# Kernel tuning notes

Measured on AMD Instinct MI355X. Metric: run time of the kernel, lower is better.

Reference implementation:

```python
import jax, jax.numpy as jnp
import numpy as np

B = 8192
D_IN = 512
UNITS = 512


def setup_inputs() -> dict:
    key = jax.random.key(0)
    ks = jax.random.split(key, 9)
    sx = 1.0 / np.sqrt(D_IN)
    sh = 1.0 / np.sqrt(UNITS)
    return {
        "input_x": jax.random.normal(ks[0], (B, D_IN), jnp.float32),
        "input_h": jax.random.normal(ks[1], (B, UNITS), jnp.float32),
        "attention_score": jax.random.uniform(ks[2], (B, 1), jnp.float32),
        "Wx_r": jax.random.normal(ks[3], (D_IN, UNITS), jnp.float32) * sx,
        "b_r": jnp.zeros((UNITS,), jnp.float32),
        "Wh_r": jax.random.normal(ks[4], (UNITS, UNITS), jnp.float32) * sh,
        "Wx_u": jax.random.normal(ks[5], (D_IN, UNITS), jnp.float32) * sx,
        "b_u": jnp.zeros((UNITS,), jnp.float32),
        "Wh_u": jax.random.normal(ks[6], (UNITS, UNITS), jnp.float32) * sh,
        "Wx_h": jax.random.normal(ks[7], (D_IN, UNITS), jnp.float32) * sx,
        "b_h": jnp.zeros((UNITS,), jnp.float32),
        "Wh_h": jax.random.normal(ks[8], (UNITS, UNITS), jnp.float32) * sh,
    }


def reference(input_x, input_h, attention_score,
              Wx_r, b_r, Wh_r,
              Wx_u, b_u, Wh_u,
              Wx_h, b_h, Wh_h):
    # reset gate: sigmoid(Dense_b(x) + Dense(h))
    r = jax.nn.sigmoid(input_x @ Wx_r + b_r + input_h @ Wh_r)
    # update gate: sigmoid(Dense_b(x) + Dense(h))
    u = jax.nn.sigmoid(input_x @ Wx_u + b_u + input_h @ Wh_u)
    # candidate: tanh(Dense_b(x) + r * Dense(h))
    cal_h = jnp.tanh(input_x @ Wx_h + b_h + r * (input_h @ Wh_h))
    # attention-modulated update and interpolation
    u_att = attention_score * u
    h = (1.0 - u_att) * input_h + u_att * cal_h
    return h
```

## Files before the change

kernel.cpp:

```cpp
#include <hip/hip_runtime.h>
#include <hip/hip_bf16.h>

typedef __bf16 bf16x8 __attribute__((ext_vector_type(8)));
typedef float f32x4 __attribute__((ext_vector_type(4)));
typedef unsigned short us8 __attribute__((ext_vector_type(8)));

#define MFMA16 __builtin_amdgcn_mfma_f32_16x16x32_bf16

__device__ __forceinline__ unsigned short f2bf(float f) {
    unsigned int u = __float_as_uint(f);
    u += 0x7fffu + ((u >> 16) & 1u);
    return (unsigned short)(u >> 16);
}

__device__ __forceinline__ void gload_lds16(const void* g, void* l) {
    __builtin_amdgcn_global_load_lds(
        (const __attribute__((address_space(1))) unsigned int*)g,
        (__attribute__((address_space(3))) unsigned int*)l, 16, 0, 0);
}

__global__ void cvt_xh_kernel(const float* __restrict__ x, const float* __restrict__ h,
                              unsigned short* __restrict__ XP, unsigned short* __restrict__ HP) {
    int c = blockIdx.x * 256 + threadIdx.x;
    const float* src = (c >> 19) ? h : x;
    unsigned short* dst = (c >> 19) ? HP : XP;
    int c2 = c & 524287;
    int mb = c2 >> 10, kb = (c2 >> 6) & 15, lane = c2 & 63;
    int r = lane & 15, ko = lane >> 4;
    const float* p = src + (size_t)(mb * 16 + r) * 512 + kb * 32 + ko * 8;
    float4 v0 = *(const float4*)p;
    float4 v1 = *(const float4*)(p + 4);
    us8 o = { f2bf(v0.x), f2bf(v0.y), f2bf(v0.z), f2bf(v0.w),
              f2bf(v1.x), f2bf(v1.y), f2bf(v1.z), f2bf(v1.w) };
    *(us8*)(dst + (size_t)c2 * 8) = o;
}

__global__ void cvt_w_kernel(const float* __restrict__ W0, const float* __restrict__ W1,
                             const float* __restrict__ W2, const float* __restrict__ W3,
                             const float* __restrict__ W4, const float* __restrict__ W5,
                             unsigned short* __restrict__ WP) {
    int c = blockIdx.x * 256 + threadIdx.x;
    int w = c >> 15;
    const float* Wsrc;
    switch (w) {
        case 0: Wsrc = W0; break;
        case 1: Wsrc = W1; break;
        case 2: Wsrc = W2; break;
        case 3: Wsrc = W3; break;
        case 4: Wsrc = W4; break;
        default: Wsrc = W5; break;
    }
    int c2 = c & 32767;
    int nb = c2 >> 10, kb = (c2 >> 6) & 15, lane = c2 & 63;
    int cc = lane & 15, ko = lane >> 4;
    int kbase = kb * 32 + ko * 8;
    us8 o;
#pragma unroll
    for (int e = 0; e < 8; ++e)
        o[e] = f2bf(Wsrc[(size_t)(kbase + e) * 512 + nb * 16 + cc]);
    *(us8*)(WP + (size_t)c * 8) = o;
}

__global__ __launch_bounds__(256, 2) void augru_mm(
    const unsigned short* __restrict__ XP,
    const unsigned short* __restrict__ HP,
    const unsigned short* __restrict__ WP,
    const float* __restrict__ b_r, const float* __restrict__ b_u, const float* __restrict__ b_h,
    const float* __restrict__ att, const float* __restrict__ h32,
    float* __restrict__ out) {
    __shared__ unsigned char sB[2][12 * 1024];

    const int t = threadIdx.x;
    const int wv = t >> 6, lane = t & 63;
    const size_t laneoff = (size_t)lane * 16;

    const int bid = blockIdx.x;
    const int W = (bid & 7) * 64 + (bid >> 3);
    const int mblk = W >> 4, nblk = W & 15;
    const int nbase = nblk * 2;
    const int mbase = mblk * 16 + wv * 4;

    f32x4 accR[4][2] = {}, accU[4][2] = {}, accXH[4][2] = {}, accHH[4][2] = {};

    const unsigned char* pX[4];
    const unsigned char* pH[4];
#pragma unroll
    for (int mf = 0; mf < 4; ++mf) {
        size_t fb = ((size_t)(mbase + mf) * 16) << 10;
        pX[mf] = (const unsigned char*)XP + fb + laneoff;
        pH[mf] = (const unsigned char*)HP + fb + laneoff;
    }

#pragma unroll
    for (int i = 0; i < 3; ++i) {
        int s = wv * 3 + i;
        int w = s >> 1, nf = s & 1;
        const unsigned char* src = (const unsigned char*)WP +
            ((((size_t)(w * 32 + nbase + nf)) * 16 + 0) << 10) + laneoff;
        gload_lds16(src, &sB[0][s << 10]);
    }
    __syncthreads();

    int buf = 0;
    for (int kb = 0; kb < 16; ++kb) {
        bf16x8 ax[4], ah[4];
#pragma unroll
        for (int mf = 0; mf < 4; ++mf) {
            ax[mf] = *(const bf16x8*)(pX[mf] + ((size_t)kb << 10));
            ah[mf] = *(const bf16x8*)(pH[mf] + ((size_t)kb << 10));
        }
        if (kb < 15) {
#pragma unroll
            for (int i = 0; i < 3; ++i) {
                int s = wv * 3 + i;
                int w = s >> 1, nf = s & 1;
                const unsigned char* src = (const unsigned char*)WP +
                    ((((size_t)(w * 32 + nbase + nf)) * 16 + (kb + 1)) << 10) + laneoff;
                gload_lds16(src, &sB[buf ^ 1][s << 10]);
            }
        }
        bf16x8 bw[6][2];
#pragma unroll
        for (int s = 0; s < 12; ++s)
            bw[s >> 1][s & 1] = *(const bf16x8*)&sB[buf][(s << 10) + laneoff];
#pragma unroll
        for (int mf = 0; mf < 4; ++mf) {
#pragma unroll
            for (int nf = 0; nf < 2; ++nf) {
                accR[mf][nf]  = MFMA16(ax[mf], bw[0][nf], accR[mf][nf], 0, 0, 0);
                accR[mf][nf]  = MFMA16(ah[mf], bw[1][nf], accR[mf][nf], 0, 0, 0);
                accU[mf][nf]  = MFMA16(ax[mf], bw[2][nf], accU[mf][nf], 0, 0, 0);
                accU[mf][nf]  = MFMA16(ah[mf], bw[3][nf], accU[mf][nf], 0, 0, 0);
                accXH[mf][nf] = MFMA16(ax[mf], bw[4][nf], accXH[mf][nf], 0, 0, 0);
                accHH[mf][nf] = MFMA16(ah[mf], bw[5][nf], accHH[mf][nf], 0, 0, 0);
            }
        }
        __syncthreads();
        buf ^= 1;
    }

    const int lr = lane & 15, lg = lane >> 4;
#pragma unroll
    for (int nf = 0; nf < 2; ++nf) {
        const int col = nblk * 32 + nf * 16 + lr;
        const float br = b_r[col], bu = b_u[col], bh = b_h[col];
#pragma unroll
        for (int mf = 0; mf < 4; ++mf) {
            const int rowb = mblk * 256 + wv * 64 + mf * 16 + lg * 4;
#pragma unroll
            for (int q = 0; q < 4; ++q) {
                const int row = rowb + q;
                float r = 1.f / (1.f + __expf(-(accR[mf][nf][q] + br)));
                float u = 1.f / (1.f + __expf(-(accU[mf][nf][q] + bu)));
                float ph = accXH[mf][nf][q] + bh + r * accHH[mf][nf][q];
                ph = fminf(fmaxf(ph, -15.f), 15.f);
                float e = __expf(2.f * ph);
                float cal = (e - 1.f) / (e + 1.f);
                float hv = h32[(size_t)row * 512 + col];
                float ua = att[row] * u;
                out[(size_t)row * 512 + col] = fmaf(ua, cal - hv, hv);
            }
        }
    }
}

extern "C" void kernel_launch(void* const* d_in, const int* in_sizes, int n_in,
                              void* d_out, int out_size, void* d_ws, size_t ws_size,
                              hipStream_t stream) {
    const float* x    = (const float*)d_in[0];
    const float* h    = (const float*)d_in[1];
    const float* att  = (const float*)d_in[2];
    const float* Wx_r = (const float*)d_in[3];
    const float* b_r  = (const float*)d_in[4];
    const float* Wh_r = (const float*)d_in[5];
    const float* Wx_u = (const float*)d_in[6];
    const float* b_u  = (const float*)d_in[7];
    const float* Wh_u = (const float*)d_in[8];
    const float* Wx_h = (const float*)d_in[9];
    const float* b_h  = (const float*)d_in[10];
    const float* Wh_h = (const float*)d_in[11];
    float* out = (float*)d_out;

    unsigned short* XP = (unsigned short*)d_ws;
    unsigned short* HP = XP + 8192 * 512;
    unsigned short* WP = HP + 8192 * 512;

    cvt_xh_kernel<<<4096, 256, 0, stream>>>(x, h, XP, HP);
    cvt_w_kernel<<<768, 256, 0, stream>>>(Wx_r, Wh_r, Wx_u, Wh_u, Wx_h, Wh_h, WP);
    augru_mm<<<512, 256, 0, stream>>>(XP, HP, WP, b_r, b_u, b_h, att, h, out);
}
```

Before: 56.23 us.

## Merge conversion kernels and software-pipeline A-fragment loads in GEMM loop

Combines the activation and weight bf16 conversion kernels into one launch, removing one kernel launch and its tail. In the main GEMM, the K loop is unrolled by two with double-buffered register A fragments, so global loads of the next X/H fragments are issued before the current MFMAs instead of right before use. This hides global load latency but raises register pressure under the 2-blocks-per-CU launch bound.

```diff
diff --git a/kernel.cpp b/kernel.cpp
--- a/kernel.cpp
+++ b/kernel.cpp
@@ -19,46 +19,47 @@
         (__attribute__((address_space(3))) unsigned int*)l, 16, 0, 0);
 }
 
-__global__ void cvt_xh_kernel(const float* __restrict__ x, const float* __restrict__ h,
-                              unsigned short* __restrict__ XP, unsigned short* __restrict__ HP) {
-    int c = blockIdx.x * 256 + threadIdx.x;
-    const float* src = (c >> 19) ? h : x;
-    unsigned short* dst = (c >> 19) ? HP : XP;
-    int c2 = c & 524287;
-    int mb = c2 >> 10, kb = (c2 >> 6) & 15, lane = c2 & 63;
-    int r = lane & 15, ko = lane >> 4;
-    const float* p = src + (size_t)(mb * 16 + r) * 512 + kb * 32 + ko * 8;
-    float4 v0 = *(const float4*)p;
-    float4 v1 = *(const float4*)(p + 4);
-    us8 o = { f2bf(v0.x), f2bf(v0.y), f2bf(v0.z), f2bf(v0.w),
-              f2bf(v1.x), f2bf(v1.y), f2bf(v1.z), f2bf(v1.w) };
-    *(us8*)(dst + (size_t)c2 * 8) = o;
-}
-
-__global__ void cvt_w_kernel(const float* __restrict__ W0, const float* __restrict__ W1,
-                             const float* __restrict__ W2, const float* __restrict__ W3,
-                             const float* __restrict__ W4, const float* __restrict__ W5,
-                             unsigned short* __restrict__ WP) {
-    int c = blockIdx.x * 256 + threadIdx.x;
-    int w = c >> 15;
-    const float* Wsrc;
-    switch (w) {
-        case 0: Wsrc = W0; break;
-        case 1: Wsrc = W1; break;
-        case 2: Wsrc = W2; break;
-        case 3: Wsrc = W3; break;
-        case 4: Wsrc = W4; break;
-        default: Wsrc = W5; break;
+__global__ void cvt_all_kernel(const float* __restrict__ x, const float* __restrict__ h,
+                               unsigned short* __restrict__ XP, unsigned short* __restrict__ HP,
+                               const float* __restrict__ W0, const float* __restrict__ W1,
+                               const float* __restrict__ W2, const float* __restrict__ W3,
+                               const float* __restrict__ W4, const float* __restrict__ W5,
+                               unsigned short* __restrict__ WP) {
+    if (blockIdx.x < 4096) {
+        int c = blockIdx.x * 256 + threadIdx.x;
+        const float* src = (c >> 19) ? h : x;
+        unsigned short* dst = (c >> 19) ? HP : XP;
+        int c2 = c & 524287;
+        int mb = c2 >> 10, kb = (c2 >> 6) & 15, lane = c2 & 63;
+        int r = lane & 15, ko = lane >> 4;
+        const float* p = src + (size_t)(mb * 16 + r) * 512 + kb * 32 + ko * 8;
+        float4 v0 = *(const float4*)p;
+        float4 v1 = *(const float4*)(p + 4);
+        us8 o = { f2bf(v0.x), f2bf(v0.y), f2bf(v0.z), f2bf(v0.w),
+                  f2bf(v1.x), f2bf(v1.y), f2bf(v1.z), f2bf(v1.w) };
+        *(us8*)(dst + (size_t)c2 * 8) = o;
+    } else {
+        int c = (blockIdx.x - 4096) * 256 + threadIdx.x;
+        int w = c >> 15;
+        const float* Wsrc;
+        switch (w) {
+            case 0: Wsrc = W0; break;
+            case 1: Wsrc = W1; break;
+            case 2: Wsrc = W2; break;
+            case 3: Wsrc = W3; break;
+            case 4: Wsrc = W4; break;
+            default: Wsrc = W5; break;
+        }
+        int c2 = c & 32767;
+        int nb = c2 >> 10, kb = (c2 >> 6) & 15, lane = c2 & 63;
+        int cc = lane & 15, ko = lane >> 4;
+        int kbase = kb * 32 + ko * 8;
+        us8 o;
+#pragma unroll
+        for (int e = 0; e < 8; ++e)
+            o[e] = f2bf(Wsrc[(size_t)(kbase + e) * 512 + nb * 16 + cc]);
+        *(us8*)(WP + (size_t)c * 8) = o;
     }
-    int c2 = c & 32767;
-    int nb = c2 >> 10, kb = (c2 >> 6) & 15, lane = c2 & 63;
-    int cc = lane & 15, ko = lane >> 4;
-    int kbase = kb * 32 + ko * 8;
-    us8 o;
-#pragma unroll
-    for (int e = 0; e < 8; ++e)
-        o[e] = f2bf(Wsrc[(size_t)(kbase + e) * 512 + nb * 16 + cc]);
-    *(us8*)(WP + (size_t)c * 8) = o;
 }
 
 __global__ __launch_bounds__(256, 2) void augru_mm(
@@ -90,53 +91,57 @@
         pX[mf] = (const unsigned char*)XP + fb + laneoff;
         pH[mf] = (const unsigned char*)HP + fb + laneoff;
     }
-
+    const unsigned char* pW[3];
+    unsigned lds_off[3];
 #pragma unroll
     for (int i = 0; i < 3; ++i) {
         int s = wv * 3 + i;
         int w = s >> 1, nf = s & 1;
-        const unsigned char* src = (const unsigned char*)WP +
-            ((((size_t)(w * 32 + nbase + nf)) * 16 + 0) << 10) + laneoff;
-        gload_lds16(src, &sB[0][s << 10]);
+        pW[i] = (const unsigned char*)WP + (((size_t)(w * 32 + nbase + nf) * 16) << 10) + laneoff;
+        lds_off[i] = s << 10;
     }
+
+#define STAGE_B(kb1, bufi) \
+    { _Pragma("unroll") for (int i = 0; i < 3; ++i) \
+        gload_lds16(pW[i] + ((size_t)(kb1) << 10), &sB[bufi][lds_off[i]]); }
+
+#define LOAD_A(kb1, slot) \
+    { _Pragma("unroll") for (int mf = 0; mf < 4; ++mf) { \
+        ax##slot[mf] = *(const bf16x8*)(pX[mf] + ((size_t)(kb1) << 10)); \
+        ah##slot[mf] = *(const bf16x8*)(pH[mf] + ((size_t)(kb1) << 10)); } }
+
+#define DO_MFMA(bufi, slot) \
+    { bf16x8 bw[6][2]; \
+      _Pragma("unroll") for (int s = 0; s < 12; ++s) \
+          bw[s >> 1][s & 1] = *(const bf16x8*)&sB[bufi][(s << 10) + laneoff]; \
+      _Pragma("unroll") for (int mf = 0; mf < 4; ++mf) { \
+          _Pragma("unroll") for (int nf = 0; nf < 2; ++nf) { \
+              accR[mf][nf]  = MFMA16(ax##slot[mf], bw[0][nf], accR[mf][nf], 0, 0, 0); \
+              accR[mf][nf]  = MFMA16(ah##slot[mf], bw[1][nf], accR[mf][nf], 0, 0, 0); \
+              accU[mf][nf]  = MFMA16(ax##slot[mf], bw[2][nf], accU[mf][nf], 0, 0, 0); \
+              accU[mf][nf]  = MFMA16(ah##slot[mf], bw[3][nf], accU[mf][nf], 0, 0, 0); \
+              accXH[mf][nf] = MFMA16(ax##slot[mf], bw[4][nf], accXH[mf][nf], 0, 0, 0); \
+              accHH[mf][nf] = MFMA16(ah##slot[mf], bw[5][nf], accHH[mf][nf], 0, 0, 0); } } }
+
+    bf16x8 ax0[4], ah0[4], ax1[4], ah1[4];
+
+    STAGE_B(0, 0)
+    LOAD_A(0, 0)
     __syncthreads();
 
-    int buf = 0;
-    for (int kb = 0; kb < 16; ++kb) {
-        bf16x8 ax[4], ah[4];
-#pragma unroll
-        for (int mf = 0; mf < 4; ++mf) {
-            ax[mf] = *(const bf16x8*)(pX[mf] + ((size_t)kb << 10));
-            ah[mf] = *(const bf16x8*)(pH[mf] + ((size_t)kb << 10));
+#pragma unroll 1
+    for (int it = 0; it < 8; ++it) {
+        const int kb0 = it * 2;
+        STAGE_B(kb0 + 1, 1)
+        LOAD_A(kb0 + 1, 1)
+        DO_MFMA(0, 0)
+        __syncthreads();
+        if (kb0 + 2 < 16) {
+            STAGE_B(kb0 + 2, 0)
+            LOAD_A(kb0 + 2, 0)
         }
-        if (kb < 15) {
-#pragma unroll
-            for (int i = 0; i < 3; ++i) {
-                int s = wv * 3 + i;
-                int w = s >> 1, nf = s & 1;
-                const unsigned char* src = (const unsigned char*)WP +
-                    ((((size_t)(w * 32 + nbase + nf)) * 16 + (kb + 1)) << 10) + laneoff;
-                gload_lds16(src, &sB[buf ^ 1][s << 10]);
-            }
-        }
-        bf16x8 bw[6][2];
-#pragma unroll
-        for (int s = 0; s < 12; ++s)
-            bw[s >> 1][s & 1] = *(const bf16x8*)&sB[buf][(s << 10) + laneoff];
-#pragma unroll
-        for (int mf = 0; mf < 4; ++mf) {
-#pragma unroll
-            for (int nf = 0; nf < 2; ++nf) {
-                accR[mf][nf]  = MFMA16(ax[mf], bw[0][nf], accR[mf][nf], 0, 0, 0);
-                accR[mf][nf]  = MFMA16(ah[mf], bw[1][nf], accR[mf][nf], 0, 0, 0);
-                accU[mf][nf]  = MFMA16(ax[mf], bw[2][nf], accU[mf][nf], 0, 0, 0);
-                accU[mf][nf]  = MFMA16(ah[mf], bw[3][nf], accU[mf][nf], 0, 0, 0);
-                accXH[mf][nf] = MFMA16(ax[mf], bw[4][nf], accXH[mf][nf], 0, 0, 0);
-                accHH[mf][nf] = MFMA16(ah[mf], bw[5][nf], accHH[mf][nf], 0, 0, 0);
-            }
-        }
+        DO_MFMA(1, 1)
         __syncthreads();
-        buf ^= 1;
     }
 
     const int lr = lane & 15, lg = lane >> 4;
@@ -162,6 +167,9 @@
             }
         }
     }
+#undef STAGE_B
+#undef LOAD_A
+#undef DO_MFMA
 }
 
 extern "C" void kernel_launch(void* const* d_in, const int* in_sizes, int n_in,
@@ -185,7 +193,7 @@
     unsigned short* HP = XP + 8192 * 512;
     unsigned short* WP = HP + 8192 * 512;
 
-    cvt_xh_kernel<<<4096, 256, 0, stream>>>(x, h, XP, HP);
-    cvt_w_kernel<<<768, 256, 0, stream>>>(Wx_r, Wh_r, Wx_u, Wh_u, Wx_h, Wh_h, WP);
+    cvt_all_kernel<<<4864, 256, 0, stream>>>(x, h, XP, HP,
+        Wx_r, Wh_r, Wx_u, Wh_u, Wx_h, Wh_h, WP);
     augru_mm<<<512, 256, 0, stream>>>(XP, HP, WP, b_r, b_u, b_h, att, h, out);
 }
```

Result: faster. 48.58 us (-13.6%).

## Merge conversion kernels and restructure GEMM into 8-wave blocks with chunked weight staging

Applied to the files above, without the earlier changes.

Fuses the activation and weight bf16 conversion kernels into one launch to remove a kernel launch gap. The main GEMM moves to 512-thread blocks where each wave handles one 16-column fragment instead of two. Weights are staged in 48KB LDS chunks covering four k-steps, replacing the per-step double buffer. MFMA issue is interleaved with LDS loads using s_setprio. Each wave now reloads the A fragments from global memory that were previously shared across two N-fragments, and the chunked staging leaves load-to-compute overlap unpipelined behind barriers.

```diff
diff --git a/kernel.cpp b/kernel.cpp
--- a/kernel.cpp
+++ b/kernel.cpp
@@ -19,147 +19,149 @@
         (__attribute__((address_space(3))) unsigned int*)l, 16, 0, 0);
 }
 
-__global__ void cvt_xh_kernel(const float* __restrict__ x, const float* __restrict__ h,
-                              unsigned short* __restrict__ XP, unsigned short* __restrict__ HP) {
-    int c = blockIdx.x * 256 + threadIdx.x;
-    const float* src = (c >> 19) ? h : x;
-    unsigned short* dst = (c >> 19) ? HP : XP;
-    int c2 = c & 524287;
-    int mb = c2 >> 10, kb = (c2 >> 6) & 15, lane = c2 & 63;
-    int r = lane & 15, ko = lane >> 4;
-    const float* p = src + (size_t)(mb * 16 + r) * 512 + kb * 32 + ko * 8;
-    float4 v0 = *(const float4*)p;
-    float4 v1 = *(const float4*)(p + 4);
-    us8 o = { f2bf(v0.x), f2bf(v0.y), f2bf(v0.z), f2bf(v0.w),
-              f2bf(v1.x), f2bf(v1.y), f2bf(v1.z), f2bf(v1.w) };
-    *(us8*)(dst + (size_t)c2 * 8) = o;
+__global__ void cvt_all_kernel(const float* __restrict__ x, const float* __restrict__ h,
+                               unsigned short* __restrict__ XP, unsigned short* __restrict__ HP,
+                               const float* __restrict__ W0, const float* __restrict__ W1,
+                               const float* __restrict__ W2, const float* __restrict__ W3,
+                               const float* __restrict__ W4, const float* __restrict__ W5,
+                               unsigned short* __restrict__ WP) {
+    if (blockIdx.x < 4096) {
+        int c = blockIdx.x * 256 + threadIdx.x;
+        const float* src = (c >> 19) ? h : x;
+        unsigned short* dst = (c >> 19) ? HP : XP;
+        int c2 = c & 524287;
+        int mb = c2 >> 10, kb = (c2 >> 6) & 15, lane = c2 & 63;
+        int r = lane & 15, ko = lane >> 4;
+        const float* p = src + (size_t)(mb * 16 + r) * 512 + kb * 32 + ko * 8;
+        float4 v0 = *(const float4*)p;
+        float4 v1 = *(const float4*)(p + 4);
+        us8 o = { f2bf(v0.x), f2bf(v0.y), f2bf(v0.z), f2bf(v0.w),
+                  f2bf(v1.x), f2bf(v1.y), f2bf(v1.z), f2bf(v1.w) };
+        *(us8*)(dst + (size_t)c2 * 8) = o;
+    } else {
+        int c = (blockIdx.x - 4096) * 256 + threadIdx.x;
+        int w = c >> 15;
+        const float* Wsrc;
+        switch (w) {
+            case 0: Wsrc = W0; break;
+            case 1: Wsrc = W1; break;
+            case 2: Wsrc = W2; break;
+            case 3: Wsrc = W3; break;
+            case 4: Wsrc = W4; break;
+            default: Wsrc = W5; break;
+        }
+        int c2 = c & 32767;
+        int nb = c2 >> 10, kb = (c2 >> 6) & 15, lane = c2 & 63;
+        int cc = lane & 15, ko = lane >> 4;
+        int kbase = kb * 32 + ko * 8;
+        us8 o;
+#pragma unroll
+        for (int e = 0; e < 8; ++e)
+            o[e] = f2bf(Wsrc[(size_t)(kbase + e) * 512 + nb * 16 + cc]);
+        *(us8*)(WP + (size_t)c * 8) = o;
+    }
 }
 
-__global__ void cvt_w_kernel(const float* __restrict__ W0, const float* __restrict__ W1,
-                             const float* __restrict__ W2, const float* __restrict__ W3,
-                             const float* __restrict__ W4, const float* __restrict__ W5,
-                             unsigned short* __restrict__ WP) {
-    int c = blockIdx.x * 256 + threadIdx.x;
-    int w = c >> 15;
-    const float* Wsrc;
-    switch (w) {
-        case 0: Wsrc = W0; break;
-        case 1: Wsrc = W1; break;
-        case 2: Wsrc = W2; break;
-        case 3: Wsrc = W3; break;
-        case 4: Wsrc = W4; break;
-        default: Wsrc = W5; break;
-    }
-    int c2 = c & 32767;
-    int nb = c2 >> 10, kb = (c2 >> 6) & 15, lane = c2 & 63;
-    int cc = lane & 15, ko = lane >> 4;
-    int kbase = kb * 32 + ko * 8;
-    us8 o;
-#pragma unroll
-    for (int e = 0; e < 8; ++e)
-        o[e] = f2bf(Wsrc[(size_t)(kbase + e) * 512 + nb * 16 + cc]);
-    *(us8*)(WP + (size_t)c * 8) = o;
-}
-
-__global__ __launch_bounds__(256, 2) void augru_mm(
+__global__ __launch_bounds__(512, 4) void augru_mm(
     const unsigned short* __restrict__ XP,
     const unsigned short* __restrict__ HP,
     const unsigned short* __restrict__ WP,
     const float* __restrict__ b_r, const float* __restrict__ b_u, const float* __restrict__ b_h,
     const float* __restrict__ att, const float* __restrict__ h32,
     float* __restrict__ out) {
-    __shared__ unsigned char sB[2][12 * 1024];
+    __shared__ unsigned char sB[48 * 1024];
 
     const int t = threadIdx.x;
     const int wv = t >> 6, lane = t & 63;
-    const size_t laneoff = (size_t)lane * 16;
+    const int laneoff = lane * 16;
 
     const int bid = blockIdx.x;
     const int W = (bid & 7) * 64 + (bid >> 3);
     const int mblk = W >> 4, nblk = W & 15;
-    const int nbase = nblk * 2;
-    const int mbase = mblk * 16 + wv * 4;
+    const int wr = wv >> 1, wc = wv & 1;
 
-    f32x4 accR[4][2] = {}, accU[4][2] = {}, accXH[4][2] = {}, accHH[4][2] = {};
+    f32x4 accR[4] = {}, accU[4] = {}, accXH[4] = {}, accHH[4] = {};
 
-    const unsigned char* pX[4];
-    const unsigned char* pH[4];
+    const unsigned char* XPb = (const unsigned char*)XP;
+    const unsigned char* HPb = (const unsigned char*)HP;
+    const unsigned char* WPb = (const unsigned char*)WP;
+
+    size_t aoff[4];
 #pragma unroll
-    for (int mf = 0; mf < 4; ++mf) {
-        size_t fb = ((size_t)(mbase + mf) * 16) << 10;
-        pX[mf] = (const unsigned char*)XP + fb + laneoff;
-        pH[mf] = (const unsigned char*)HP + fb + laneoff;
+    for (int mf = 0; mf < 4; ++mf)
+        aoff[mf] = ((size_t)((mblk * 16 + wr * 4 + mf) * 16) << 10) + laneoff;
+
+    const unsigned char* wsrc[6];
+    unsigned sdst[6];
+#pragma unroll
+    for (int i = 0; i < 6; ++i) {
+        int fid = wv + i * 8;
+        int s = fid >> 3, nf = (fid >> 2) & 1, kbi = fid & 3;
+        wsrc[i] = WPb + ((size_t)(s * 512 + (nblk * 2 + nf) * 16 + kbi) << 10) + laneoff;
+        sdst[i] = (unsigned)fid << 10;
     }
 
 #pragma unroll
-    for (int i = 0; i < 3; ++i) {
-        int s = wv * 3 + i;
-        int w = s >> 1, nf = s & 1;
-        const unsigned char* src = (const unsigned char*)WP +
-            ((((size_t)(w * 32 + nbase + nf)) * 16 + 0) << 10) + laneoff;
-        gload_lds16(src, &sB[0][s << 10]);
-    }
-    __syncthreads();
+    for (int c = 0; c < 4; ++c) {
+        __syncthreads();
+#pragma unroll
+        for (int i = 0; i < 6; ++i)
+            gload_lds16(wsrc[i] + ((size_t)c << 12), &sB[sdst[i]]);
+        __syncthreads();
 
-    int buf = 0;
-    for (int kb = 0; kb < 16; ++kb) {
-        bf16x8 ax[4], ah[4];
 #pragma unroll
-        for (int mf = 0; mf < 4; ++mf) {
-            ax[mf] = *(const bf16x8*)(pX[mf] + ((size_t)kb << 10));
-            ah[mf] = *(const bf16x8*)(pH[mf] + ((size_t)kb << 10));
+        for (int kbi = 0; kbi < 4; ++kbi) {
+            const int kb = c * 4 + kbi;
+            const size_t koff = (size_t)kb << 10;
+            bf16x8 ax[4], ah[4];
+#pragma unroll
+            for (int mf = 0; mf < 4; ++mf) ax[mf] = *(const bf16x8*)(XPb + aoff[mf] + koff);
+            const unsigned rb = (unsigned)((wc * 4 + kbi) << 10) + laneoff;
+            bf16x8 b0 = *(const bf16x8*)&sB[0 * 8192 + rb];
+            bf16x8 b2 = *(const bf16x8*)&sB[2 * 8192 + rb];
+            bf16x8 b4 = *(const bf16x8*)&sB[4 * 8192 + rb];
+#pragma unroll
+            for (int mf = 0; mf < 4; ++mf) ah[mf] = *(const bf16x8*)(HPb + aoff[mf] + koff);
+            __builtin_amdgcn_s_setprio(1);
+#pragma unroll
+            for (int mf = 0; mf < 4; ++mf) {
+                accR[mf]  = MFMA16(ax[mf], b0, accR[mf], 0, 0, 0);
+                accU[mf]  = MFMA16(ax[mf], b2, accU[mf], 0, 0, 0);
+                accXH[mf] = MFMA16(ax[mf], b4, accXH[mf], 0, 0, 0);
+            }
+            __builtin_amdgcn_s_setprio(0);
+            bf16x8 b1 = *(const bf16x8*)&sB[1 * 8192 + rb];
+            bf16x8 b3 = *(const bf16x8*)&sB[3 * 8192 + rb];
+            bf16x8 b5 = *(const bf16x8*)&sB[5 * 8192 + rb];
+            __builtin_amdgcn_s_setprio(1);
+#pragma unroll
+            for (int mf = 0; mf < 4; ++mf) {
+                accR[mf]  = MFMA16(ah[mf], b1, accR[mf], 0, 0, 0);
+                accU[mf]  = MFMA16(ah[mf], b3, accU[mf], 0, 0, 0);
+                accHH[mf] = MFMA16(ah[mf], b5, accHH[mf], 0, 0, 0);
+            }
+            __builtin_amdgcn_s_setprio(0);
         }
-        if (kb < 15) {
-#pragma unroll
-            for (int i = 0; i < 3; ++i) {
-                int s = wv * 3 + i;
-                int w = s >> 1, nf = s & 1;
-                const unsigned char* src = (const unsigned char*)WP +
-                    ((((size_t)(w * 32 + nbase + nf)) * 16 + (kb + 1)) << 10) + laneoff;
-                gload_lds16(src, &sB[buf ^ 1][s << 10]);
-            }
-        }
-        bf16x8 bw[6][2];
-#pragma unroll
-        for (int s = 0; s < 12; ++s)
-            bw[s >> 1][s & 1] = *(const bf16x8*)&sB[buf][(s << 10) + laneoff];
-#pragma unroll
-        for (int mf = 0; mf < 4; ++mf) {
-#pragma unroll
-            for (int nf = 0; nf < 2; ++nf) {
-                accR[mf][nf]  = MFMA16(ax[mf], bw[0][nf], accR[mf][nf], 0, 0, 0);
-                accR[mf][nf]  = MFMA16(ah[mf], bw[1][nf], accR[mf][nf], 0, 0, 0);
-                accU[mf][nf]  = MFMA16(ax[mf], bw[2][nf], accU[mf][nf], 0, 0, 0);
-                accU[mf][nf]  = MFMA16(ah[mf], bw[3][nf], accU[mf][nf], 0, 0, 0);
-                accXH[mf][nf] = MFMA16(ax[mf], bw[4][nf], accXH[mf][nf], 0, 0, 0);
-                accHH[mf][nf] = MFMA16(ah[mf], bw[5][nf], accHH[mf][nf], 0, 0, 0);
-            }
-        }
-        __syncthreads();
-        buf ^= 1;
     }
 
     const int lr = lane & 15, lg = lane >> 4;
+    const int col = nblk * 32 + wc * 16 + lr;
+    const float br = b_r[col], bu = b_u[col], bh = b_h[col];
 #pragma unroll
-    for (int nf = 0; nf < 2; ++nf) {
-        const int col = nblk * 32 + nf * 16 + lr;
-        const float br = b_r[col], bu = b_u[col], bh = b_h[col];
+    for (int mf = 0; mf < 4; ++mf) {
+        const int rowb = mblk * 256 + wr * 64 + mf * 16 + lg * 4;
 #pragma unroll
-        for (int mf = 0; mf < 4; ++mf) {
-            const int rowb = mblk * 256 + wv * 64 + mf * 16 + lg * 4;
-#pragma unroll
-            for (int q = 0; q < 4; ++q) {
-                const int row = rowb + q;
-                float r = 1.f / (1.f + __expf(-(accR[mf][nf][q] + br)));
-                float u = 1.f / (1.f + __expf(-(accU[mf][nf][q] + bu)));
-                float ph = accXH[mf][nf][q] + bh + r * accHH[mf][nf][q];
-                ph = fminf(fmaxf(ph, -15.f), 15.f);
-                float e = __expf(2.f * ph);
-                float cal = (e - 1.f) / (e + 1.f);
-                float hv = h32[(size_t)row * 512 + col];
-                float ua = att[row] * u;
-                out[(size_t)row * 512 + col] = fmaf(ua, cal - hv, hv);
-            }
+        for (int q = 0; q < 4; ++q) {
+            const int row = rowb + q;
+            float r = 1.f / (1.f + __expf(-(accR[mf][q] + br)));
+            float u = 1.f / (1.f + __expf(-(accU[mf][q] + bu)));
+            float ph = accXH[mf][q] + bh + r * accHH[mf][q];
+            ph = fminf(fmaxf(ph, -15.f), 15.f);
+            float e = __expf(2.f * ph);
+            float cal = (e - 1.f) / (e + 1.f);
+            float hv = h32[(size_t)row * 512 + col];
+            float ua = att[row] * u;
+            out[(size_t)row * 512 + col] = fmaf(ua, cal - hv, hv);
         }
     }
 }
@@ -185,7 +187,7 @@
     unsigned short* HP = XP + 8192 * 512;
     unsigned short* WP = HP + 8192 * 512;
 
-    cvt_xh_kernel<<<4096, 256, 0, stream>>>(x, h, XP, HP);
-    cvt_w_kernel<<<768, 256, 0, stream>>>(Wx_r, Wh_r, Wx_u, Wh_u, Wx_h, Wh_h, WP);
-    augru_mm<<<512, 256, 0, stream>>>(XP, HP, WP, b_r, b_u, b_h, att, h, out);
+    cvt_all_kernel<<<4864, 256, 0, stream>>>(x, h, XP, HP,
+        Wx_r, Wh_r, Wx_u, Wh_u, Wx_h, Wh_h, WP);
+    augru_mm<<<512, 512, 0, stream>>>(XP, HP, WP, b_r, b_u, b_h, att, h, out);
 }
```

After: 52.41 us. -6.8%, faster.
